# Kernel optimization log

Hardware: AMD Instinct MI355X
Metric: run time of the kernel (lower is better)

The kernel has to match this reference:

```python
import jax, jax.numpy as jnp
import numpy as np

NUM_HEADS = 12
SCALE = 0.125  # (C // num_heads) ** -0.5 = 64 ** -0.5


def setup_inputs() -> dict:
    key = jax.random.key(0)
    k1, k2, k3, k4, k5 = jax.random.split(key, 5)
    B, N, C = 8, 1024, 768
    x = jax.random.normal(k1, (B, N, C), dtype=jnp.float32)
    qkv_w = jax.random.normal(k2, (3 * C, C), dtype=jnp.float32) * (C ** -0.5)
    qkv_b = jax.random.normal(k3, (3 * C,), dtype=jnp.float32) * 0.02
    proj_w = jax.random.normal(k4, (C, C), dtype=jnp.float32) * (C ** -0.5)
    proj_b = jax.random.normal(k5, (C,), dtype=jnp.float32) * 0.02
    return {"x": x, "qkv_w": qkv_w, "qkv_b": qkv_b,
            "proj_w": proj_w, "proj_b": proj_b, "H": 32, "W": 32}


def reference(x, qkv_w, qkv_b, proj_w, proj_b, H, W):
    B, N, C = x.shape
    hd = C // NUM_HEADS
    # qkv: [B, N, 3C] -> [3, B, heads, N, hd]
    qkv = (x @ qkv_w.T + qkv_b).reshape(B, N, 3, NUM_HEADS, hd)
    qkv = jnp.transpose(qkv, (2, 0, 3, 1, 4))
    q, k, v = qkv[0], qkv[1], qkv[2]
    # attention scores [B, heads, N, N]
    attn = jnp.einsum('bhnd,bhmd->bhnm', q, k) * SCALE
    attn = jax.nn.softmax(attn, axis=-1)
    # attn_drop / proj_drop are identity in eval mode
    out = jnp.einsum('bhnm,bhmd->bhnd', attn, v)
    out = jnp.transpose(out, (0, 2, 1, 3)).reshape(B, N, C)
    out = out @ proj_w.T + proj_b
    return out
```

## Files before the change

kernel.cpp:

```cpp
#include <hip/hip_runtime.h>
#include <math.h>

#define NSEQ  1024
#define CDIM  768
#define NH    12
#define HD    64
#define QS    6291456
#define EXPC  0.18033688011112042f

typedef __bf16 bf16x8 __attribute__((ext_vector_type(8)));
typedef float  f32x4  __attribute__((ext_vector_type(4)));

__device__ __forceinline__ unsigned short f2bf(float f) {
    union { float f; unsigned u; } v; v.f = f;
    unsigned r = v.u + 0x7FFFu + ((v.u >> 16) & 1u);
    return (unsigned short)(r >> 16);
}

#if __has_builtin(__builtin_amdgcn_cvt_pk_bf16_f32)
typedef __bf16 bf16x2 __attribute__((ext_vector_type(2)));
__device__ __forceinline__ void store_p4(unsigned short* pr, int row16,
                                         float p0, float p1, float p2, float p3) {
    union { bf16x2 v; unsigned u; } a, b;
    a.v = __builtin_amdgcn_cvt_pk_bf16_f32(p0, p1);
    b.v = __builtin_amdgcn_cvt_pk_bf16_f32(p2, p3);
    pr[row16]      = (unsigned short)(a.u);
    pr[16 + row16] = (unsigned short)(a.u >> 16);
    pr[32 + row16] = (unsigned short)(b.u);
    pr[48 + row16] = (unsigned short)(b.u >> 16);
}
#else
__device__ __forceinline__ void store_p4(unsigned short* pr, int row16,
                                         float p0, float p1, float p2, float p3) {
    pr[row16]      = f2bf(p0);
    pr[16 + row16] = f2bf(p1);
    pr[32 + row16] = f2bf(p2);
    pr[48 + row16] = f2bf(p3);
}
#endif

__device__ __forceinline__ void gld_lds16(const unsigned short* g, unsigned short* l) {
    __builtin_amdgcn_global_load_lds(
        (const __attribute__((address_space(1))) void*)g,
        (__attribute__((address_space(3))) void*)l, 16, 0, 0);
}

__global__ __launch_bounds__(256) void cvt_all(const float* __restrict__ x,
                                               const float* __restrict__ w1,
                                               const float* __restrict__ w2,
                                               unsigned short* __restrict__ xb,
                                               unsigned short* __restrict__ w1b,
                                               unsigned short* __restrict__ w2b,
                                               int n0, int n1, int n2) {
    int i = (blockIdx.x * 256 + threadIdx.x) * 4;
    const float* s; unsigned short* d; int off;
    if (i < n0)           { s = x;  d = xb;  off = i; }
    else if (i < n0 + n1) { s = w1; d = w1b; off = i - n0; }
    else if (i < n0 + n1 + n2) { s = w2; d = w2b; off = i - n0 - n1; }
    else return;
    float4 v = *(const float4*)(s + off);
    ushort4 o;
    o.x = f2bf(v.x); o.y = f2bf(v.y); o.z = f2bf(v.z); o.w = f2bf(v.w);
    *(ushort4*)(d + off) = o;
}

template <int MODE>
__global__ __launch_bounds__(256) void mfma_gemm_bt(const unsigned short* __restrict__ A,
                                                    const unsigned short* __restrict__ Bw,
                                                    const float* __restrict__ bias,
                                                    void* __restrict__ outp,
                                                    int M, int N, int K) {
    __shared__ unsigned short smem[2 * 128 * 64];
    unsigned short* As = smem;
    unsigned short* Bs = smem + 128 * 64;

    const int tid = threadIdx.x;
    const int wave = tid >> 6, lane = tid & 63;
    const int row16 = lane & 15, quad = lane >> 4;
    const int wm = (wave >> 1) * 64, wn = (wave & 1) * 64;
    const int m0 = blockIdx.x * 128, n0 = blockIdx.y * 128;

    f32x4 acc[4][4];
#pragma unroll
    for (int i = 0; i < 4; ++i)
#pragma unroll
        for (int j = 0; j < 4; ++j) acc[i][j] = (f32x4){0.f, 0.f, 0.f, 0.f};

    for (int k0 = 0; k0 < K; k0 += 64) {
        __syncthreads();
#pragma unroll
        for (int i = 0; i < 4; ++i) {
            const int flat = (tid + i * 256) * 8;
            const int row = flat >> 6, col = flat & 63;
            gld_lds16(&A[(size_t)(m0 + row) * K + k0 + col], &As[i * 2048 + wave * 512]);
            gld_lds16(&Bw[(size_t)(n0 + row) * K + k0 + col], &Bs[i * 2048 + wave * 512]);
        }
        __syncthreads();
#pragma unroll
        for (int kst = 0; kst < 2; ++kst) {
            bf16x8 af[4], bfr[4];
#pragma unroll
            for (int mt = 0; mt < 4; ++mt)
                af[mt] = *(const bf16x8*)&As[(wm + mt * 16 + row16) * 64 + kst * 32 + quad * 8];
#pragma unroll
            for (int nt = 0; nt < 4; ++nt)
                bfr[nt] = *(const bf16x8*)&Bs[(wn + nt * 16 + row16) * 64 + kst * 32 + quad * 8];
#pragma unroll
            for (int mt = 0; mt < 4; ++mt)
#pragma unroll
                for (int nt = 0; nt < 4; ++nt)
                    acc[mt][nt] = __builtin_amdgcn_mfma_f32_16x16x32_bf16(af[mt], bfr[nt], acc[mt][nt], 0, 0, 0);
        }
    }

    float bias4[4];
#pragma unroll
    for (int nt = 0; nt < 4; ++nt) bias4[nt] = bias[n0 + wn + nt * 16 + row16];

    if (MODE == 0) {
#pragma unroll
        for (int mt = 0; mt < 4; ++mt)
#pragma unroll
            for (int nt = 0; nt < 4; ++nt)
#pragma unroll
                for (int r = 0; r < 4; ++r) {
                    int grow = m0 + wm + mt * 16 + quad * 4 + r;
                    int gcol = n0 + wn + nt * 16 + row16;
                    ((float*)outp)[(size_t)grow * N + gcol] = acc[mt][nt][r] + bias4[nt];
                }
    } else {
        unsigned short* qkvb = (unsigned short*)outp;
        __syncthreads();
#pragma unroll
        for (int mt = 0; mt < 4; ++mt)
#pragma unroll
            for (int nt = 0; nt < 4; ++nt)
#pragma unroll
                for (int r = 0; r < 4; ++r)
                    smem[(wm + mt * 16 + quad * 4 + r) * 128 + wn + nt * 16 + row16] =
                        f2bf(acc[mt][nt][r] + bias4[nt]);
        __syncthreads();
#pragma unroll
        for (int i = 0; i < 8; ++i) {
            int u4 = i * 256 + tid;
            int row = u4 >> 4;
            int c8 = u4 & 15;
            int grow = m0 + row;
            int gcol = n0 + c8 * 8;
            int t = gcol / CDIM;
            int rr = gcol - t * CDIM;
            int h = rr >> 6, d = rr & 63;
            int b = grow >> 10, n = grow & 1023;
            *(uint4*)&qkvb[(size_t)t * QS + ((((size_t)b * NH + h) << 10) + n) * 64 + d] =
                *(const uint4*)&smem[row * 128 + c8 * 8];
        }
    }
}

__global__ __launch_bounds__(256, 4) void attn_mfma(const unsigned short* __restrict__ qkv,
                                                    unsigned short* __restrict__ abuf) {
    __shared__ unsigned short Ks[64 * 72];
    __shared__ unsigned short Vt[64 * 72];
    __shared__ unsigned short Ps[4][32 * 72];

    const int tid = threadIdx.x;
    const int wave = tid >> 6, lane = tid & 63;
    const int row16 = lane & 15, quad = lane >> 4;
    const int bid = blockIdx.x;
    const int xcd = bid & 7;
    const int local = bid >> 3;
    const int bh = xcd * 12 + (local >> 3);
    const int qt = local & 7;

    const unsigned short* Qg = qkv + (size_t)bh * NSEQ * HD + (size_t)qt * 128 * HD;
    const unsigned short* Kg = qkv + (size_t)QS + (size_t)bh * NSEQ * HD;
    const unsigned short* Vg = qkv + (size_t)2 * QS + (size_t)bh * NSEQ * HD;

    bf16x8 aq[2][2];
#pragma unroll
    for (int mt = 0; mt < 2; ++mt)
#pragma unroll
        for (int kst = 0; kst < 2; ++kst)
            aq[mt][kst] = *(const bf16x8*)&Qg[(size_t)(wave * 32 + mt * 16 + row16) * 64 +
                                              kst * 32 + quad * 8];

    f32x4 o[2][4];
    float l_i[2][4];
#pragma unroll
    for (int mt = 0; mt < 2; ++mt)
#pragma unroll
        for (int j = 0; j < 4; ++j) {
            o[mt][j] = (f32x4){0.f, 0.f, 0.f, 0.f};
            l_i[mt][j] = 0.f;
        }

    const int krow0 = (tid * 8) >> 6,  kcol0 = (tid * 8) & 63;
    const int krow1 = ((tid + 256) * 8) >> 6, kcol1 = ((tid + 256) * 8) & 63;
    const int kpair = tid & 31;
    const int colc = tid >> 5;

    uint4 ka = *(const uint4*)&Kg[(size_t)krow0 * 64 + kcol0];
    uint4 kb = *(const uint4*)&Kg[(size_t)krow1 * 64 + kcol1];
    uint4 va = *(const uint4*)&Vg[(size_t)(2 * kpair) * 64 + colc * 8];
    uint4 vb = *(const uint4*)&Vg[(size_t)(2 * kpair + 1) * 64 + colc * 8];

    for (int kt = 0; kt < 16; ++kt) {
        __syncthreads();
        *(uint4*)&Ks[krow0 * 72 + kcol0] = ka;
        *(uint4*)&Ks[krow1 * 72 + kcol1] = kb;
        {
            const unsigned short* a16 = (const unsigned short*)&va;
            const unsigned short* b16 = (const unsigned short*)&vb;
            unsigned int* vt32 = (unsigned int*)Vt;
#pragma unroll
            for (int j = 0; j < 8; ++j)
                vt32[(colc * 8 + j) * 36 + kpair] =
                    (unsigned int)a16[j] | ((unsigned int)b16[j] << 16);
        }
        __syncthreads();

        if (kt < 15) {
            const unsigned short* kn = Kg + (size_t)(kt + 1) * 64 * 64;
            const unsigned short* vn = Vg + (size_t)(kt + 1) * 64 * 64;
            ka = *(const uint4*)&kn[(size_t)krow0 * 64 + kcol0];
            kb = *(const uint4*)&kn[(size_t)krow1 * 64 + kcol1];
            va = *(const uint4*)&vn[(size_t)(2 * kpair) * 64 + colc * 8];
            vb = *(const uint4*)&vn[(size_t)(2 * kpair + 1) * 64 + colc * 8];
        }

        f32x4 s[2][4];
#pragma unroll
        for (int mt = 0; mt < 2; ++mt)
#pragma unroll
            for (int nt = 0; nt < 4; ++nt) s[mt][nt] = (f32x4){0.f, 0.f, 0.f, 0.f};
#pragma unroll
        for (int kst = 0; kst < 2; ++kst) {
            bf16x8 bk[4];
#pragma unroll
            for (int nt = 0; nt < 4; ++nt)
                bk[nt] = *(const bf16x8*)&Ks[(nt * 16 + row16) * 72 + kst * 32 + quad * 8];
#pragma unroll
            for (int mt = 0; mt < 2; ++mt)
#pragma unroll
                for (int nt = 0; nt < 4; ++nt)
                    s[mt][nt] = __builtin_amdgcn_mfma_f32_16x16x32_bf16(aq[mt][kst], bk[nt], s[mt][nt], 0, 0, 0);
        }

#pragma unroll
        for (int mt = 0; mt < 2; ++mt)
#pragma unroll
            for (int r = 0; r < 4; ++r) {
                float p0 = __builtin_amdgcn_exp2f(s[mt][0][r] * EXPC);
                float p1 = __builtin_amdgcn_exp2f(s[mt][1][r] * EXPC);
                float p2 = __builtin_amdgcn_exp2f(s[mt][2][r] * EXPC);
                float p3 = __builtin_amdgcn_exp2f(s[mt][3][r] * EXPC);
                l_i[mt][r] += (p0 + p1) + (p2 + p3);
                store_p4(&Ps[wave][(mt * 16 + quad * 4 + r) * 72], row16, p0, p1, p2, p3);
            }

#pragma unroll
        for (int kst = 0; kst < 2; ++kst) {
            bf16x8 ap[2], bv[4];
#pragma unroll
            for (int mt = 0; mt < 2; ++mt)
                ap[mt] = *(const bf16x8*)&Ps[wave][(mt * 16 + row16) * 72 + kst * 32 + quad * 8];
#pragma unroll
            for (int dt = 0; dt < 4; ++dt)
                bv[dt] = *(const bf16x8*)&Vt[(dt * 16 + row16) * 72 + kst * 32 + quad * 8];
#pragma unroll
            for (int mt = 0; mt < 2; ++mt)
#pragma unroll
                for (int dt = 0; dt < 4; ++dt)
                    o[mt][dt] = __builtin_amdgcn_mfma_f32_16x16x32_bf16(ap[mt], bv[dt], o[mt][dt], 0, 0, 0);
        }
    }

    const int b = bh / NH, h = bh - b * NH;
#pragma unroll
    for (int mt = 0; mt < 2; ++mt)
#pragma unroll
        for (int r = 0; r < 4; ++r) {
            float l = l_i[mt][r];
            l += __shfl_xor(l, 1);
            l += __shfl_xor(l, 2);
            l += __shfl_xor(l, 4);
            l += __shfl_xor(l, 8);
            float inv = 1.f / l;
            int n = qt * 128 + wave * 32 + mt * 16 + quad * 4 + r;
            size_t base = ((size_t)(b * NSEQ + n)) * CDIM + h * HD;
#pragma unroll
            for (int dt = 0; dt < 4; ++dt)
                abuf[base + dt * 16 + row16] = f2bf(o[mt][dt][r] * inv);
        }
}

extern "C" void kernel_launch(void* const* d_in, const int* in_sizes, int n_in,
                              void* d_out, int out_size, void* d_ws, size_t ws_size,
                              hipStream_t stream) {
    const float* x      = (const float*)d_in[0];
    const float* qkv_w  = (const float*)d_in[1];
    const float* qkv_b  = (const float*)d_in[2];
    const float* proj_w = (const float*)d_in[3];
    const float* proj_b = (const float*)d_in[4];
    float* out = (float*)d_out;

    const int M = 8 * NSEQ;
    unsigned short* ws = (unsigned short*)d_ws;
    unsigned short* xb   = ws;
    unsigned short* wq   = xb + (size_t)M * CDIM;
    unsigned short* wp   = wq + (size_t)3 * CDIM * CDIM;
    unsigned short* qkvb = wp + (size_t)CDIM * CDIM;
    unsigned short* ab   = qkvb + (size_t)3 * QS;

    const int nx = M * CDIM, nq = 3 * CDIM * CDIM, np = CDIM * CDIM;
    cvt_all<<<(nx + nq + np) / 1024, 256, 0, stream>>>(x, qkv_w, proj_w, xb, wq, wp,
                                                       nx, nq, np);

    mfma_gemm_bt<1><<<dim3(M / 128, (3 * CDIM) / 128), 256, 0, stream>>>(
        xb, wq, qkv_b, qkvb, M, 3 * CDIM, CDIM);

    attn_mfma<<<dim3(8 * NH * (NSEQ / 128)), 256, 0, stream>>>(qkvb, ab);

    mfma_gemm_bt<0><<<dim3(M / 128, CDIM / 128), 256, 0, stream>>>(
        ab, wp, proj_b, out, M, CDIM, CDIM);
}
```

Measured before the change: 219.8 us.

## Double-buffer GEMM LDS tiles with K-step 32 to overlap loads and MFMA

```diff
diff --git a/kernel.cpp b/kernel.cpp
--- a/kernel.cpp
+++ b/kernel.cpp
@@ -70,9 +70,7 @@
                                                     const float* __restrict__ bias,
                                                     void* __restrict__ outp,
                                                     int M, int N, int K) {
-    __shared__ unsigned short smem[2 * 128 * 64];
-    unsigned short* As = smem;
-    unsigned short* Bs = smem + 128 * 64;
+    __shared__ unsigned short smem[4 * 128 * 32];
 
     const int tid = threadIdx.x;
     const int wave = tid >> 6, lane = tid & 63;
@@ -80,37 +78,44 @@
     const int wm = (wave >> 1) * 64, wn = (wave & 1) * 64;
     const int m0 = blockIdx.x * 128, n0 = blockIdx.y * 128;
 
+    const int srow0 = (tid * 8) >> 5,         scol0 = (tid * 8) & 31;
+    const int srow1 = ((tid + 256) * 8) >> 5, scol1 = ((tid + 256) * 8) & 31;
+
     f32x4 acc[4][4];
 #pragma unroll
     for (int i = 0; i < 4; ++i)
 #pragma unroll
         for (int j = 0; j < 4; ++j) acc[i][j] = (f32x4){0.f, 0.f, 0.f, 0.f};
 
-    for (int k0 = 0; k0 < K; k0 += 64) {
-        __syncthreads();
-#pragma unroll
-        for (int i = 0; i < 4; ++i) {
-            const int flat = (tid + i * 256) * 8;
-            const int row = flat >> 6, col = flat & 63;
-            gld_lds16(&A[(size_t)(m0 + row) * K + k0 + col], &As[i * 2048 + wave * 512]);
-            gld_lds16(&Bw[(size_t)(n0 + row) * K + k0 + col], &Bs[i * 2048 + wave * 512]);
-        }
-        __syncthreads();
-#pragma unroll
-        for (int kst = 0; kst < 2; ++kst) {
-            bf16x8 af[4], bfr[4];
-#pragma unroll
-            for (int mt = 0; mt < 4; ++mt)
-                af[mt] = *(const bf16x8*)&As[(wm + mt * 16 + row16) * 64 + kst * 32 + quad * 8];
+    gld_lds16(&A[(size_t)(m0 + srow0) * K + scol0], &smem[wave * 512]);
+    gld_lds16(&A[(size_t)(m0 + srow1) * K + scol1], &smem[2048 + wave * 512]);
+    gld_lds16(&Bw[(size_t)(n0 + srow0) * K + scol0], &smem[8192 + wave * 512]);
+    gld_lds16(&Bw[(size_t)(n0 + srow1) * K + scol1], &smem[8192 + 2048 + wave * 512]);
+
+    const int nk = K / 32;
+    for (int ki = 0; ki < nk; ++ki) {
+        const int co = (ki & 1) * 4096;
+        const int no = 4096 - co;
+        __syncthreads();
+        if (ki + 1 < nk) {
+            const int k0 = (ki + 1) * 32;
+            gld_lds16(&A[(size_t)(m0 + srow0) * K + k0 + scol0], &smem[no + wave * 512]);
+            gld_lds16(&A[(size_t)(m0 + srow1) * K + k0 + scol1], &smem[no + 2048 + wave * 512]);
+            gld_lds16(&Bw[(size_t)(n0 + srow0) * K + k0 + scol0], &smem[8192 + no + wave * 512]);
+            gld_lds16(&Bw[(size_t)(n0 + srow1) * K + k0 + scol1], &smem[8192 + no + 2048 + wave * 512]);
+        }
+        bf16x8 af[4], bfr[4];
+#pragma unroll
+        for (int mt = 0; mt < 4; ++mt)
+            af[mt] = *(const bf16x8*)&smem[co + (wm + mt * 16 + row16) * 32 + quad * 8];
+#pragma unroll
+        for (int nt = 0; nt < 4; ++nt)
+            bfr[nt] = *(const bf16x8*)&smem[8192 + co + (wn + nt * 16 + row16) * 32 + quad * 8];
+#pragma unroll
+        for (int mt = 0; mt < 4; ++mt)
 #pragma unroll
             for (int nt = 0; nt < 4; ++nt)
-                bfr[nt] = *(const bf16x8*)&Bs[(wn + nt * 16 + row16) * 64 + kst * 32 + quad * 8];
-#pragma unroll
-            for (int mt = 0; mt < 4; ++mt)
-#pragma unroll
-                for (int nt = 0; nt < 4; ++nt)
-                    acc[mt][nt] = __builtin_amdgcn_mfma_f32_16x16x32_bf16(af[mt], bfr[nt], acc[mt][nt], 0, 0, 0);
-        }
+                acc[mt][nt] = __builtin_amdgcn_mfma_f32_16x16x32_bf16(af[mt], bfr[nt], acc[mt][nt], 0, 0, 0);
     }
 
     float bias4[4];
```

Result: faster. 195.6 us (-11.0%).
